# Performance work log

Hardware: AMD Instinct MI355X
Metric: run time of the kernel (lower is better)

## Reference

```python
import jax, jax.numpy as jnp
import numpy as np

DIM = 1024
NUM_HEADS = 32
HEAD_DIM = 32
T = 2048
SCALE = 0.12
ROT_BASE = HEAD_DIM * 4  # Rotary(head_dim, max_seq_len, head_dim*4)
RMS_EPS = 1.1920929e-07  # torch float32 finfo eps (F.rms_norm default)


def _rms_norm(x):
    ms = jnp.mean(jnp.square(x), axis=-1, keepdims=True)
    return x * jax.lax.rsqrt(ms + RMS_EPS)


def _rotary_tables(seq_len):
    # modded-nanogpt half-truncated rotary: frequencies on first quarter, zeros on second
    quarter = HEAD_DIM // 4
    af = (1.0 / ROT_BASE) ** jnp.linspace(0.0, 1.0, quarter, dtype=jnp.float32)
    af = jnp.concatenate([af, jnp.zeros(quarter, dtype=jnp.float32)])  # [hd/2]
    theta = jnp.arange(seq_len, dtype=jnp.float32)[:, None] * af[None, :]  # [T, hd/2]
    return jnp.cos(theta), jnp.sin(theta)


def _apply_rotary(x, cos, sin):
    # x: [B, T, H, hd]; cos/sin: [T, hd/2]
    x1, x2 = jnp.split(x, 2, axis=-1)
    c = cos[None, :, None, :]
    s = sin[None, :, None, :]
    y1 = x1 * c + x2 * s
    y2 = -x1 * s + x2 * c
    return jnp.concatenate([y1, y2], axis=-1)


def setup_inputs() -> dict:
    key = jax.random.key(0)
    k1, k2, k3, k4 = jax.random.split(key, 4)
    std = 0.5 * DIM ** (-0.5)
    bound = (3.0 ** 0.5) * std
    x = jax.random.normal(k1, (1, T, DIM), dtype=jnp.float32)
    ve = jax.random.normal(k2, (1, T, NUM_HEADS * HEAD_DIM), dtype=jnp.float32)
    qkv_w = jax.random.uniform(k3, (3, NUM_HEADS * HEAD_DIM, DIM), dtype=jnp.float32,
                               minval=-bound, maxval=bound)
    lambdas = jnp.array([0.5, 0.5], dtype=jnp.float32)
    # original zero-inits c_proj; use small random so output/grads are nontrivial
    c_proj_w = jax.random.normal(k4, (DIM, NUM_HEADS * HEAD_DIM), dtype=jnp.float32) * 0.02
    return {"x": x, "ve": ve, "qkv_w": qkv_w, "lambdas": lambdas, "c_proj_w": c_proj_w}


def reference(x, ve, qkv_w, lambdas, c_proj_w):
    B, T_, D = x.shape
    H, hd = NUM_HEADS, HEAD_DIM
    # fused QKV projection: F.linear(x, qkv_w.flatten(end_dim=1))
    w = qkv_w.reshape(3 * H * hd, D)
    qkv = jnp.einsum('btd,ed->bte', x, w).reshape(B, T_, 3 * H, hd)
    q, k, v = jnp.split(qkv, 3, axis=2)  # each [B, T, H, hd]
    q = _rms_norm(q)
    k = _rms_norm(k)
    cos, sin = _rotary_tables(T_)
    q = _apply_rotary(q, cos, sin)
    k = _apply_rotary(k, cos, sin)
    v = lambdas[0] * v + lambdas[1] * ve.reshape(B, T_, H, hd)
    # causal attention with fixed scale 0.12
    scores = jnp.einsum('bqhd,bkhd->bhqk', q, k) * SCALE
    causal = jnp.tril(jnp.ones((T_, T_), dtype=bool))
    scores = jnp.where(causal[None, None, :, :], scores, -jnp.inf)
    attn = jax.nn.softmax(scores, axis=-1)
    y = jnp.einsum('bhqk,bkhd->bqhd', attn, v).reshape(B, T_, H * hd)
    return jnp.einsum('bte,de->btd', y, c_proj_w)
```

## Files before the change

kernel.cpp:

```cpp
#include <hip/hip_runtime.h>
#include <hip/hip_bf16.h>

#define NHEADS 32
#define HD_ 32
#define TSEQ 2048
#define SCALE_ 0.12f
#define LOG2E_ 1.44269504088896f
#define RMS_EPS_ 1.1920929e-07f

typedef unsigned short ushort_t;
typedef __bf16 bf16_t;
typedef __attribute__((ext_vector_type(8))) bf16_t bf16x8;
typedef __attribute__((ext_vector_type(4))) float f32x4;
typedef __attribute__((ext_vector_type(8))) unsigned short u16x8;

__device__ __forceinline__ ushort_t f2bfn(float f){
    __hip_bfloat16 b = __float2bfloat16(f);
    return *reinterpret_cast<ushort_t*>(&b);
}
__device__ __forceinline__ float bf2f(ushort_t s){
    union { unsigned u; float f; } v; v.u = ((unsigned)s) << 16;
    return v.f;
}
__device__ __forceinline__ float fexp2(float x){
#if __has_builtin(__builtin_amdgcn_exp2f)
    return __builtin_amdgcn_exp2f(x);
#else
    return exp2f(x);
#endif
}
__device__ __forceinline__ void gld16(const void* g, void* l){
    __builtin_amdgcn_global_load_lds(
        (const __attribute__((address_space(1))) unsigned int*)g,
        (__attribute__((address_space(3))) unsigned int*)l,
        16, 0, 0);
}

__global__ __launch_bounds__(256) void k_prep(const float* __restrict__ x,
                                              const float* __restrict__ qkw,
                                              const float* __restrict__ cpw,
                                              ushort_t* __restrict__ xb,
                                              ushort_t* __restrict__ wb,
                                              ushort_t* __restrict__ cpb,
                                              float* __restrict__ cost,
                                              float* __restrict__ sint)
{
    const int n1 = TSEQ * 1024 / 4, n2 = 3 * 1024 * 1024 / 4, n3 = 1024 * 1024 / 4;
    int i = blockIdx.x * 256 + threadIdx.x;
    if (i < n1 + n2 + n3){
        const float* src; ushort_t* dst; int j = i;
        if (j < n1){ src = x; dst = xb; }
        else if (j < n1 + n2){ j -= n1; src = qkw; dst = wb; }
        else { j -= n1 + n2; src = cpw; dst = cpb; }
        float4 v = ((const float4*)src)[j];
        ushort4 o;
        o.x = f2bfn(v.x); o.y = f2bfn(v.y); o.z = f2bfn(v.z); o.w = f2bfn(v.w);
        ((ushort4*)dst)[j] = o;
    } else {
        int g = i - (n1 + n2 + n3);
        if (g < TSEQ * 16){
            int t = g >> 4, ii = g & 15;
            float c = 1.0f, s = 0.0f;
            if (ii < 8){
                float af = powf(1.0f / 128.0f, (float)ii * (1.0f / 7.0f));
                sincosf((float)t * af, &s, &c);
            }
            cost[g] = c; sint[g] = s;
        }
    }
}

__global__ __launch_bounds__(256, 3) void k_gemm128(const ushort_t* __restrict__ A,
                                                    const ushort_t* __restrict__ B,
                                                    ushort_t* __restrict__ C,
                                                    int M, int N, int K)
{
    __shared__ __align__(16) ushort_t As[2][128 * 32];
    __shared__ __align__(16) ushort_t Bs[2][128 * 32];
    const int tid = threadIdx.x;
    const int lane = tid & 63;
    const int w = tid >> 6;
    const int wr = w >> 1, wc = w & 1;
    const int l15 = lane & 15, hi = lane >> 4;
    const int m0 = blockIdx.y * 128, n0 = blockIdx.x * 128;
    const int srow = lane >> 2, scol = (lane & 3) * 8;

    f32x4 acc[4][4] = {};

    auto stage = [&](int k0, int buf){
        #pragma unroll
        for (int i = 0; i < 2; ++i){
            int c = w * 2 + i;
            gld16(&A[(size_t)(m0 + c * 16 + srow) * K + k0 + scol], &As[buf][c * 512]);
            gld16(&B[(size_t)(n0 + c * 16 + srow) * K + k0 + scol], &Bs[buf][c * 512]);
        }
    };

    stage(0, 0);
    int cur = 0;
    for (int k0 = 0; k0 < K; k0 += 32){
        __syncthreads();
        if (k0 + 32 < K) stage(k0 + 32, cur ^ 1);
        bf16x8 af[4], bfr[4];
        #pragma unroll
        for (int mi = 0; mi < 4; ++mi)
            af[mi] = *(const bf16x8*)&As[cur][(wr * 64 + mi * 16 + l15) * 32 + hi * 8];
        #pragma unroll
        for (int ni = 0; ni < 4; ++ni)
            bfr[ni] = *(const bf16x8*)&Bs[cur][(wc * 64 + ni * 16 + l15) * 32 + hi * 8];
        #pragma unroll
        for (int mi = 0; mi < 4; ++mi)
            #pragma unroll
            for (int ni = 0; ni < 4; ++ni)
                acc[mi][ni] = __builtin_amdgcn_mfma_f32_16x16x32_bf16(af[mi], bfr[ni], acc[mi][ni], 0, 0, 0);
        cur ^= 1;
    }

    #pragma unroll
    for (int mi = 0; mi < 4; ++mi)
        #pragma unroll
        for (int ni = 0; ni < 4; ++ni)
            #pragma unroll
            for (int r = 0; r < 4; ++r){
                int row = m0 + wr * 64 + mi * 16 + hi * 4 + r;
                int col = n0 + wc * 64 + ni * 16 + l15;
                C[(size_t)row * N + col] = f2bfn(acc[mi][ni][r]);
            }
}

__global__ __launch_bounds__(256) void k_gemm_out(const ushort_t* __restrict__ A,
                                                  const ushort_t* __restrict__ B,
                                                  float* __restrict__ C,
                                                  int M, int N, int K)
{
    __shared__ __align__(16) ushort_t As[2][64 * 64];
    __shared__ __align__(16) ushort_t Bs[2][64 * 64];
    const int tid = threadIdx.x;
    const int lane = tid & 63;
    const int w = tid >> 6;
    const int wr = w >> 1, wc = w & 1;
    const int l15 = lane & 15, hi = lane >> 4;
    const int m0 = blockIdx.y * 64, n0 = blockIdx.x * 64;
    const int srow = lane >> 3, scol = (lane & 7) * 8;

    f32x4 acc[2][2] = {};

    auto stage = [&](int k0, int buf){
        #pragma unroll
        for (int i = 0; i < 2; ++i){
            int c = w * 2 + i;
            gld16(&A[(size_t)(m0 + c * 8 + srow) * K + k0 + scol], &As[buf][c * 512]);
            gld16(&B[(size_t)(n0 + c * 8 + srow) * K + k0 + scol], &Bs[buf][c * 512]);
        }
    };

    stage(0, 0);
    int cur = 0;
    for (int k0 = 0; k0 < K; k0 += 64){
        __syncthreads();
        if (k0 + 64 < K) stage(k0 + 64, cur ^ 1);
        bf16x8 af[2][2], bfr[2][2];
        #pragma unroll
        for (int mi = 0; mi < 2; ++mi)
            #pragma unroll
            for (int sub = 0; sub < 2; ++sub)
                af[mi][sub] = *(const bf16x8*)&As[cur][(wr * 32 + mi * 16 + l15) * 64 + sub * 32 + hi * 8];
        #pragma unroll
        for (int ni = 0; ni < 2; ++ni)
            #pragma unroll
            for (int sub = 0; sub < 2; ++sub)
                bfr[ni][sub] = *(const bf16x8*)&Bs[cur][(wc * 32 + ni * 16 + l15) * 64 + sub * 32 + hi * 8];
        #pragma unroll
        for (int sub = 0; sub < 2; ++sub)
            #pragma unroll
            for (int mi = 0; mi < 2; ++mi)
                #pragma unroll
                for (int ni = 0; ni < 2; ++ni)
                    acc[mi][ni] = __builtin_amdgcn_mfma_f32_16x16x32_bf16(af[mi][sub], bfr[ni][sub], acc[mi][ni], 0, 0, 0);
        cur ^= 1;
    }

    #pragma unroll
    for (int mi = 0; mi < 2; ++mi)
        #pragma unroll
        for (int ni = 0; ni < 2; ++ni)
            #pragma unroll
            for (int r = 0; r < 4; ++r){
                int row = m0 + wr * 32 + mi * 16 + hi * 4 + r;
                int col = n0 + wc * 32 + ni * 16 + l15;
                C[(size_t)row * N + col] = acc[mi][ni][r];
            }
}

__global__ __launch_bounds__(256) void k_fuse(const ushort_t* __restrict__ qkvb,
                                              const float* __restrict__ ve,
                                              const float* __restrict__ lam,
                                              const float* __restrict__ cost,
                                              const float* __restrict__ sint,
                                              ushort_t* __restrict__ qb,
                                              ushort_t* __restrict__ kb,
                                              ushort_t* __restrict__ vtb)
{
    const int h  = blockIdx.y;
    const int t0 = blockIdx.x * 64;
    const int tid = threadIdx.x;
    const int tl = tid >> 2;
    const int dg = tid & 3;
    const int t  = t0 + tl;

    __shared__ __align__(16) float vtile[32 * 65];

    float cs[8], sn[8];
    #pragma unroll
    for (int j = 0; j < 8; ++j){
        int ci = (dg * 8 + j) & 15;
        cs[j] = cost[t * 16 + ci];
        sn[j] = sint[t * 16 + ci];
    }
    const float sgn = (dg < 2) ? 1.0f : -1.0f;

    #pragma unroll
    for (int which = 0; which < 2; ++which){
        u16x8 raw = *(const u16x8*)&qkvb[(size_t)t * 3072 + which * 1024 + h * 32 + dg * 8];
        float v[8];
        float ss = 0.0f;
        #pragma unroll
        for (int j = 0; j < 8; ++j){ v[j] = bf2f(raw[j]); ss += v[j] * v[j]; }
        ss += __shfl_xor(ss, 1);
        ss += __shfl_xor(ss, 2);
        const float inv = rsqrtf(ss * (1.0f / 32.0f) + RMS_EPS_);
        const float scl = (which == 0) ? SCALE_ * LOG2E_ : 1.0f;
        u16x8 o;
        #pragma unroll
        for (int j = 0; j < 8; ++j){
            float nv = v[j] * inv;
            float p  = __shfl_xor(nv, 2);
            o[j] = f2bfn((nv * cs[j] + sgn * p * sn[j]) * scl);
        }
        ushort_t* dst = (which == 0) ? qb : kb;
        *(u16x8*)&dst[((size_t)h * TSEQ + t) * 32 + dg * 8] = o;
    }

    const float l0 = lam[0], l1 = lam[1];
    {
        u16x8 raw = *(const u16x8*)&qkvb[(size_t)t * 3072 + 2048 + h * 32 + dg * 8];
        const float4* vep = (const float4*)&ve[(size_t)t * 1024 + h * 32 + dg * 8];
        float4 a = vep[0], b = vep[1];
        float vef[8] = {a.x, a.y, a.z, a.w, b.x, b.y, b.z, b.w};
        #pragma unroll
        for (int j = 0; j < 8; ++j)
            vtile[(dg * 8 + j) * 65 + tl] = l0 * bf2f(raw[j]) + l1 * vef[j];
    }
    __syncthreads();
    {
        const int d = tid >> 3, jj = tid & 7;
        u16x8 o;
        #pragma unroll
        for (int e = 0; e < 8; ++e)
            o[e] = f2bfn(vtile[d * 65 + jj * 8 + e]);
        *(u16x8*)&vtb[((size_t)h * HD_ + d) * TSEQ + t0 + jj * 8] = o;
    }
}

template<bool MASK>
__device__ __forceinline__ void chain_step(const bf16x8* kf, const bf16x8* vv0, const bf16x8* vv1,
                                           ushort_t* pb, const bf16x8& qf,
                                           int kb0, int qrow, int l15, int hi,
                                           f32x4& a0, f32x4& a1, float& lp)
{
    f32x4 s[4];
    __builtin_amdgcn_s_setprio(1);
    #pragma unroll
    for (int ni = 0; ni < 4; ++ni){
        f32x4 z = {0.f, 0.f, 0.f, 0.f};
        s[ni] = __builtin_amdgcn_mfma_f32_16x16x32_bf16(kf[ni], qf, z, 0, 0, 0);
    }
    __builtin_amdgcn_s_setprio(0);
    if (MASK){
        const int relc = qrow - kb0 - 4 * hi;
        #pragma unroll
        for (int ni = 0; ni < 4; ++ni)
            #pragma unroll
            for (int r = 0; r < 4; ++r)
                if (16 * ni + r > relc) s[ni][r] = -1e30f;
    }
    float ps = 0.f;
    #pragma unroll
    for (int ni = 0; ni < 4; ++ni)
        #pragma unroll
        for (int r = 0; r < 4; ++r){
            float p = fexp2(s[ni][r]);
            s[ni][r] = p;
            ps += p;
        }
    lp += ps;
    #pragma unroll
    for (int ni = 0; ni < 4; ++ni){
        ushort4 pk;
        pk.x = f2bfn(s[ni][0]); pk.y = f2bfn(s[ni][1]);
        pk.z = f2bfn(s[ni][2]); pk.w = f2bfn(s[ni][3]);
        *(ushort4*)&pb[l15 * 72 + ni * 16 + hi * 4] = pk;
    }
    __builtin_amdgcn_s_setprio(1);
    #pragma unroll
    for (int kk = 0; kk < 2; ++kk){
        bf16x8 pf = *(const bf16x8*)&pb[l15 * 72 + kk * 32 + hi * 8];
        a0 = __builtin_amdgcn_mfma_f32_16x16x32_bf16(vv0[kk], pf, a0, 0, 0, 0);
        a1 = __builtin_amdgcn_mfma_f32_16x16x32_bf16(vv1[kk], pf, a1, 0, 0, 0);
    }
    __builtin_amdgcn_s_setprio(0);
}

__global__ __launch_bounds__(256) void k_attn(const ushort_t* __restrict__ qb,
                                              const ushort_t* __restrict__ kb,
                                              const ushort_t* __restrict__ vtb,
                                              ushort_t* __restrict__ yb)
{
    const int bid = blockIdx.x;
    const int xcd = bid & 7, idx = bid >> 3;
    const int h = xcd * 4 + (idx >> 4);
    const int b = idx & 15;
    const int tid = threadIdx.x;
    const int w = tid >> 6, lane = tid & 63;
    const int l15 = lane & 15, hi = lane >> 4;

    __shared__ __align__(16) ushort_t Kbuf[2][128 * 32];
    __shared__ __align__(16) ushort_t Vbuf[2][32 * 128];
    __shared__ __align__(16) ushort_t Pbuf[4][16 * 72];

    const ushort_t* kb_h = kb + (size_t)h * TSEQ * HD_;
    const ushort_t* vt_h = vtb + (size_t)h * HD_ * TSEQ;
    const ushort_t* qb_h = qb + (size_t)h * TSEQ * HD_;

    const int qtA = b, qtB = 31 - b;
    const int qwA = qtA * 64 + w * 16, qwB = qtB * 64 + w * 16;
    const bf16x8 qfA = *(const bf16x8*)&qb_h[(size_t)(qwA + l15) * 32 + hi * 8];
    const bf16x8 qfB = *(const bf16x8*)&qb_h[(size_t)(qwB + l15) * 32 + hi * 8];

    const int kck0 = w * 2;
    auto stage = [&](int bs, int buf){
        const int kb0 = bs * 128;
        #pragma unroll
        for (int i = 0; i < 2; ++i){
            int c = kck0 + i;
            int krow = c * 16 + (lane >> 2);
            gld16(&kb_h[(size_t)(kb0 + krow) * 32 + (lane & 3) * 8], &Kbuf[buf][c * 512]);
            int vrow = c * 4 + (lane >> 4);
            int vj = (lane & 15) ^ (vrow & 7);
            gld16(&vt_h[(size_t)vrow * TSEQ + kb0 + vj * 8], &Vbuf[buf][c * 512]);
        }
    };

    f32x4 a0A = {0.f,0.f,0.f,0.f}, a1A = a0A, a0B = a0A, a1B = a0A;
    float lpA = 0.f, lpB = 0.f;
    ushort_t* pb = &Pbuf[w][0];

    const int nA = qtA + 1, nB = qtB + 1;
    const int NB2 = (nB + 1) >> 1;

    stage(0, 0);
    int cur = 0;
    for (int bs = 0; bs < NB2; ++bs){
        __syncthreads();
        if (bs + 1 < NB2) stage(bs + 1, cur ^ 1);
        #pragma unroll
        for (int sub = 0; sub < 2; ++sub){
            const int kt = bs * 2 + sub;
            if (kt >= nB) break;
            const int kb0 = kt * 64;
            bf16x8 kf[4], vv0[2], vv1[2];
            #pragma unroll
            for (int ni = 0; ni < 4; ++ni)
                kf[ni] = *(const bf16x8*)&Kbuf[cur][(sub * 64 + ni * 16 + l15) * 32 + hi * 8];
            #pragma unroll
            for (int kk = 0; kk < 2; ++kk){
                int sl = sub * 8 + kk * 4 + hi;
                vv0[kk] = *(const bf16x8*)&Vbuf[cur][l15 * 128 + (sl ^ (l15 & 7)) * 8];
                vv1[kk] = *(const bf16x8*)&Vbuf[cur][(16 + l15) * 128 + (sl ^ (l15 & 7)) * 8];
            }
            if (kt < qtB)
                chain_step<false>(kf, vv0, vv1, pb, qfB, kb0, qwB + l15, l15, hi, a0B, a1B, lpB);
            else
                chain_step<true >(kf, vv0, vv1, pb, qfB, kb0, qwB + l15, l15, hi, a0B, a1B, lpB);
            if (kt < qtA)
                chain_step<false>(kf, vv0, vv1, pb, qfA, kb0, qwA + l15, l15, hi, a0A, a1A, lpA);
            else if (kt == qtA)
                chain_step<true >(kf, vv0, vv1, pb, qfA, kb0, qwA + l15, l15, hi, a0A, a1A, lpA);
        }
        cur ^= 1;
    }

    #pragma unroll
    for (int which = 0; which < 2; ++which){
        f32x4 a0 = which ? a0B : a0A;
        f32x4 a1 = which ? a1B : a1A;
        float lp = which ? lpB : lpA;
        int qw = which ? qwB : qwA;
        lp += __shfl_xor(lp, 16);
        lp += __shfl_xor(lp, 32);
        float inv = 1.0f / lp;
        ushort4 o0, o1;
        o0.x = f2bfn(a0[0]*inv); o0.y = f2bfn(a0[1]*inv);
        o0.z = f2bfn(a0[2]*inv); o0.w = f2bfn(a0[3]*inv);
        o1.x = f2bfn(a1[0]*inv); o1.y = f2bfn(a1[1]*inv);
        o1.z = f2bfn(a1[2]*inv); o1.w = f2bfn(a1[3]*inv);
        size_t base = (size_t)(qw + l15) * 1024 + h * 32;
        *(ushort4*)&yb[base + hi * 4]      = o0;
        *(ushort4*)&yb[base + 16 + hi * 4] = o1;
    }
}

extern "C" void kernel_launch(void* const* d_in, const int* in_sizes, int n_in,
                              void* d_out, int out_size, void* d_ws, size_t ws_size,
                              hipStream_t stream)
{
    const float* x   = (const float*)d_in[0];
    const float* ve  = (const float*)d_in[1];
    const float* qkw = (const float*)d_in[2];
    const float* lam = (const float*)d_in[3];
    const float* cpw = (const float*)d_in[4];

    char* ws = (char*)d_ws;
    size_t o = 0;
    auto take = [&](size_t bytes) -> char* {
        char* p = ws + o; o += (bytes + 255) & ~(size_t)255; return p;
    };
    ushort_t* xb   = (ushort_t*)take((size_t)TSEQ * 1024 * 2);
    ushort_t* wb   = (ushort_t*)take((size_t)3072 * 1024 * 2);
    ushort_t* cpb  = (ushort_t*)take((size_t)1024 * 1024 * 2);
    ushort_t* qkvb = (ushort_t*)take((size_t)TSEQ * 3072 * 2);
    float*    cost = (float*)take((size_t)TSEQ * 16 * 4);
    float*    sint = (float*)take((size_t)TSEQ * 16 * 4);
    ushort_t* qb   = (ushort_t*)take((size_t)NHEADS * TSEQ * HD_ * 2);
    ushort_t* kb   = (ushort_t*)take((size_t)NHEADS * TSEQ * HD_ * 2 + 8192);
    ushort_t* vtb  = (ushort_t*)take((size_t)NHEADS * HD_ * TSEQ * 2 + 8192);
    ushort_t* yb   = xb;

    const int prep_items = (TSEQ * 1024 + 3 * 1024 * 1024 + 1024 * 1024) / 4 + TSEQ * 16;
    k_prep<<<(prep_items + 255) / 256, 256, 0, stream>>>(x, qkw, cpw, xb, wb, cpb, cost, sint);
    k_gemm128<<<dim3(3072 / 128, TSEQ / 128), 256, 0, stream>>>(xb, wb, qkvb, TSEQ, 3072, 1024);
    k_fuse<<<dim3(TSEQ / 64, NHEADS), 256, 0, stream>>>(qkvb, ve, lam, cost, sint, qb, kb, vtb);
    k_attn<<<512, 256, 0, stream>>>(qb, kb, vtb, yb);
    k_gemm_out<<<dim3(1024 / 64, TSEQ / 64), 256, 0, stream>>>(yb, cpb, (float*)d_out, TSEQ, 1024, 1024);
}
```

Measured before the change: 159.3 us.

## Fuse QK RMS-norm, rotary and V mixing/transpose into QKV GEMM epilogue

```diff
diff --git a/kernel.cpp b/kernel.cpp
--- a/kernel.cpp
+++ b/kernel.cpp
@@ -70,30 +70,38 @@
     }
 }
 
-__global__ __launch_bounds__(256, 3) void k_gemm128(const ushort_t* __restrict__ A,
-                                                    const ushort_t* __restrict__ B,
-                                                    ushort_t* __restrict__ C,
-                                                    int M, int N, int K)
-{
+__global__ __launch_bounds__(256, 3) void k_gemm_qkv(const ushort_t* __restrict__ A,
+                                                     const ushort_t* __restrict__ B,
+                                                     const float* __restrict__ ve,
+                                                     const float* __restrict__ lam,
+                                                     const float* __restrict__ cost,
+                                                     const float* __restrict__ sint,
+                                                     ushort_t* __restrict__ qb,
+                                                     ushort_t* __restrict__ kbuf,
+                                                     ushort_t* __restrict__ vtb)
+{
+    const int K = 1024;
     __shared__ __align__(16) ushort_t As[2][128 * 32];
-    __shared__ __align__(16) ushort_t Bs[2][128 * 32];
+    __shared__ __align__(16) ushort_t Bs[2][64 * 32];
     const int tid = threadIdx.x;
     const int lane = tid & 63;
     const int w = tid >> 6;
     const int wr = w >> 1, wc = w & 1;
     const int l15 = lane & 15, hi = lane >> 4;
-    const int m0 = blockIdx.y * 128, n0 = blockIdx.x * 128;
+    const int m0 = blockIdx.y * 128, n0 = blockIdx.x * 64;
+    const int sec = n0 >> 10;
+    const int h = ((n0 & 1023) >> 5) + wc;
     const int srow = lane >> 2, scol = (lane & 3) * 8;
 
-    f32x4 acc[4][4] = {};
+    f32x4 acc[4][2] = {};
 
     auto stage = [&](int k0, int buf){
         #pragma unroll
         for (int i = 0; i < 2; ++i){
-            int c = w * 2 + i;
+            int c = w + i * 4;
             gld16(&A[(size_t)(m0 + c * 16 + srow) * K + k0 + scol], &As[buf][c * 512]);
-            gld16(&B[(size_t)(n0 + c * 16 + srow) * K + k0 + scol], &Bs[buf][c * 512]);
-        }
+        }
+        gld16(&B[(size_t)(n0 + w * 16 + srow) * K + k0 + scol], &Bs[buf][w * 512]);
     };
 
     stage(0, 0);
@@ -101,31 +109,75 @@
     for (int k0 = 0; k0 < K; k0 += 32){
         __syncthreads();
         if (k0 + 32 < K) stage(k0 + 32, cur ^ 1);
-        bf16x8 af[4], bfr[4];
+        bf16x8 af[4], bfr[2];
         #pragma unroll
         for (int mi = 0; mi < 4; ++mi)
             af[mi] = *(const bf16x8*)&As[cur][(wr * 64 + mi * 16 + l15) * 32 + hi * 8];
         #pragma unroll
-        for (int ni = 0; ni < 4; ++ni)
-            bfr[ni] = *(const bf16x8*)&Bs[cur][(wc * 64 + ni * 16 + l15) * 32 + hi * 8];
+        for (int ni = 0; ni < 2; ++ni)
+            bfr[ni] = *(const bf16x8*)&Bs[cur][(wc * 32 + ni * 16 + l15) * 32 + hi * 8];
         #pragma unroll
         for (int mi = 0; mi < 4; ++mi)
             #pragma unroll
-            for (int ni = 0; ni < 4; ++ni)
+            for (int ni = 0; ni < 2; ++ni)
                 acc[mi][ni] = __builtin_amdgcn_mfma_f32_16x16x32_bf16(af[mi], bfr[ni], acc[mi][ni], 0, 0, 0);
         cur ^= 1;
     }
 
-    #pragma unroll
-    for (int mi = 0; mi < 4; ++mi)
-        #pragma unroll
-        for (int ni = 0; ni < 4; ++ni)
+    if (sec < 2){
+        ushort_t* dst = (sec == 0) ? qb : kbuf;
+        const float qscl = (sec == 0) ? SCALE_ * LOG2E_ : 1.0f;
+        #pragma unroll
+        for (int mi = 0; mi < 4; ++mi){
             #pragma unroll
             for (int r = 0; r < 4; ++r){
-                int row = m0 + wr * 64 + mi * 16 + hi * 4 + r;
-                int col = n0 + wc * 64 + ni * 16 + l15;
-                C[(size_t)row * N + col] = f2bfn(acc[mi][ni][r]);
+                const int t = m0 + wr * 64 + mi * 16 + hi * 4 + r;
+                float v0 = acc[mi][0][r], v1 = acc[mi][1][r];
+                float ss = v0 * v0 + v1 * v1;
+                ss += __shfl_xor(ss, 1);
+                ss += __shfl_xor(ss, 2);
+                ss += __shfl_xor(ss, 4);
+                ss += __shfl_xor(ss, 8);
+                const float inv = rsqrtf(ss * (1.0f / 32.0f) + RMS_EPS_);
+                const float c = cost[t * 16 + l15], s = sint[t * 16 + l15];
+                const float n0v = v0 * inv, n1v = v1 * inv;
+                const float o0 = (n0v * c + n1v * s) * qscl;
+                const float o1 = (n1v * c - n0v * s) * qscl;
+                size_t base = ((size_t)h * TSEQ + t) * 32;
+                dst[base + l15]      = f2bfn(o0);
+                dst[base + 16 + l15] = f2bfn(o1);
             }
+        }
+    } else {
+        const float l0 = lam[0], l1 = lam[1];
+        __syncthreads();
+        ushort_t* vt = &As[0][0] + w * 2048;
+        #pragma unroll
+        for (int ni = 0; ni < 2; ++ni){
+            const int d = ni * 16 + l15;
+            #pragma unroll
+            for (int mi = 0; mi < 4; ++mi){
+                #pragma unroll
+                for (int r = 0; r < 4; ++r){
+                    const int t = m0 + wr * 64 + mi * 16 + hi * 4 + r;
+                    const int tl = mi * 16 + hi * 4 + r;
+                    float vef = ve[(size_t)t * 1024 + h * 32 + d];
+                    float ov = l0 * acc[mi][ni][r] + l1 * vef;
+                    const int g = (tl >> 3) ^ (d & 7);
+                    vt[d * 64 + g * 8 + (tl & 7)] = f2bfn(ov);
+                }
+            }
+        }
+        __syncthreads();
+        const int tc = lane & 7;
+        #pragma unroll
+        for (int p = 0; p < 4; ++p){
+            const int d = p * 8 + (lane >> 3);
+            const int g = tc ^ (d & 7);
+            u16x8 o = *(const u16x8*)&vt[d * 64 + g * 8];
+            *(u16x8*)&vtb[((size_t)h * HD_ + d) * TSEQ + m0 + wr * 64 + tc * 8] = o;
+        }
+    }
 }
 
 __global__ __launch_bounds__(256) void k_gemm_out(const ushort_t* __restrict__ A,
@@ -192,76 +244,6 @@
             }
 }
 
-__global__ __launch_bounds__(256) void k_fuse(const ushort_t* __restrict__ qkvb,
-                                              const float* __restrict__ ve,
-                                              const float* __restrict__ lam,
-                                              const float* __restrict__ cost,
-                                              const float* __restrict__ sint,
-                                              ushort_t* __restrict__ qb,
-                                              ushort_t* __restrict__ kb,
-                                              ushort_t* __restrict__ vtb)
-{
-    const int h  = blockIdx.y;
-    const int t0 = blockIdx.x * 64;
-    const int tid = threadIdx.x;
-    const int tl = tid >> 2;
-    const int dg = tid & 3;
-    const int t  = t0 + tl;
-
-    __shared__ __align__(16) float vtile[32 * 65];
-
-    float cs[8], sn[8];
-    #pragma unroll
-    for (int j = 0; j < 8; ++j){
-        int ci = (dg * 8 + j) & 15;
-        cs[j] = cost[t * 16 + ci];
-        sn[j] = sint[t * 16 + ci];
-    }
-    const float sgn = (dg < 2) ? 1.0f : -1.0f;
-
-    #pragma unroll
-    for (int which = 0; which < 2; ++which){
-        u16x8 raw = *(const u16x8*)&qkvb[(size_t)t * 3072 + which * 1024 + h * 32 + dg * 8];
-        float v[8];
-        float ss = 0.0f;
-        #pragma unroll
-        for (int j = 0; j < 8; ++j){ v[j] = bf2f(raw[j]); ss += v[j] * v[j]; }
-        ss += __shfl_xor(ss, 1);
-        ss += __shfl_xor(ss, 2);
-        const float inv = rsqrtf(ss * (1.0f / 32.0f) + RMS_EPS_);
-        const float scl = (which == 0) ? SCALE_ * LOG2E_ : 1.0f;
-        u16x8 o;
-        #pragma unroll
-        for (int j = 0; j < 8; ++j){
-            float nv = v[j] * inv;
-            float p  = __shfl_xor(nv, 2);
-            o[j] = f2bfn((nv * cs[j] + sgn * p * sn[j]) * scl);
-        }
-        ushort_t* dst = (which == 0) ? qb : kb;
-        *(u16x8*)&dst[((size_t)h * TSEQ + t) * 32 + dg * 8] = o;
-    }
-
-    const float l0 = lam[0], l1 = lam[1];
-    {
-        u16x8 raw = *(const u16x8*)&qkvb[(size_t)t * 3072 + 2048 + h * 32 + dg * 8];
-        const float4* vep = (const float4*)&ve[(size_t)t * 1024 + h * 32 + dg * 8];
-        float4 a = vep[0], b = vep[1];
-        float vef[8] = {a.x, a.y, a.z, a.w, b.x, b.y, b.z, b.w};
-        #pragma unroll
-        for (int j = 0; j < 8; ++j)
-            vtile[(dg * 8 + j) * 65 + tl] = l0 * bf2f(raw[j]) + l1 * vef[j];
-    }
-    __syncthreads();
-    {
-        const int d = tid >> 3, jj = tid & 7;
-        u16x8 o;
-        #pragma unroll
-        for (int e = 0; e < 8; ++e)
-            o[e] = f2bfn(vtile[d * 65 + jj * 8 + e]);
-        *(u16x8*)&vtb[((size_t)h * HD_ + d) * TSEQ + t0 + jj * 8] = o;
-    }
-}
-
 template<bool MASK>
 __device__ __forceinline__ void chain_step(const bf16x8* kf, const bf16x8* vv0, const bf16x8* vv1,
                                            ushort_t* pb, const bf16x8& qf,
@@ -355,7 +337,7 @@
     float lpA = 0.f, lpB = 0.f;
     ushort_t* pb = &Pbuf[w][0];
 
-    const int nA = qtA + 1, nB = qtB + 1;
+    const int nB = qtB + 1;
     const int NB2 = (nB + 1) >> 1;
 
     stage(0, 0);
@@ -428,7 +410,6 @@
     ushort_t* xb   = (ushort_t*)take((size_t)TSEQ * 1024 * 2);
     ushort_t* wb   = (ushort_t*)take((size_t)3072 * 1024 * 2);
     ushort_t* cpb  = (ushort_t*)take((size_t)1024 * 1024 * 2);
-    ushort_t* qkvb = (ushort_t*)take((size_t)TSEQ * 3072 * 2);
     float*    cost = (float*)take((size_t)TSEQ * 16 * 4);
     float*    sint = (float*)take((size_t)TSEQ * 16 * 4);
     ushort_t* qb   = (ushort_t*)take((size_t)NHEADS * TSEQ * HD_ * 2);
@@ -438,8 +419,7 @@
 
     const int prep_items = (TSEQ * 1024 + 3 * 1024 * 1024 + 1024 * 1024) / 4 + TSEQ * 16;
     k_prep<<<(prep_items + 255) / 256, 256, 0, stream>>>(x, qkw, cpw, xb, wb, cpb, cost, sint);
-    k_gemm128<<<dim3(3072 / 128, TSEQ / 128), 256, 0, stream>>>(xb, wb, qkvb, TSEQ, 3072, 1024);
-    k_fuse<<<dim3(TSEQ / 64, NHEADS), 256, 0, stream>>>(qkvb, ve, lam, cost, sint, qb, kb, vtb);
+    k_gemm_qkv<<<dim3(48, 16), 256, 0, stream>>>(xb, wb, ve, lam, cost, sint, qb, kb, vtb);
     k_attn<<<512, 256, 0, stream>>>(qb, kb, vtb, yb);
     k_gemm_out<<<dim3(1024 / 64, TSEQ / 64), 256, 0, stream>>>(yb, cpb, (float*)d_out, TSEQ, 1024, 1024);
 }
```

Result: faster. 153.2 us (-3.8%).
